# Kernel tuning notes

Hardware: AMD Instinct MI355X
Metric: run time of the kernel (lower is better)

## Reference

```python
import jax, jax.numpy as jnp
import numpy as np

ALPHA = 0.2  # LeakyReLU negative slope
EPS = 1e-6


def gam(x):
    # relu6(x+3)/3 + eps
    return jnp.clip(x + 3.0, 0.0, 6.0) / 3.0 + EPS


def leaky(x):
    return jnp.where(x >= 0, x, ALPHA * x)


def relu_bt(x):
    # threshold at detached inf-norm of input: min(leaky_relu(x), ||x||_inf)
    t = jax.lax.stop_gradient(jnp.max(jnp.abs(x)))
    return jnp.minimum(leaky(x), t)


def setup_inputs() -> dict:
    key = jax.random.key(0)
    ks = jax.random.split(key, 8)
    N, E, Din, Dout = 100000, 1600000, 256, 64
    return {
        "input": jax.random.normal(ks[0], (N, Din), dtype=jnp.float32),
        "edge": jax.random.randint(ks[1], (2, E), 0, N, dtype=jnp.int32),
        "W_high": jax.random.normal(ks[2], (Din, Dout), dtype=jnp.float32) * 0.06,
        "W_low": jax.random.normal(ks[3], (Din, Dout), dtype=jnp.float32) * 0.06,
        "a_high": jax.random.normal(ks[4], (1, 4 * Dout), dtype=jnp.float32) * 0.09,
        "a_low": jax.random.normal(ks[5], (1, 4 * Dout), dtype=jnp.float32) * 0.09,
        "c_high": jax.random.uniform(ks[6], (1, 1), dtype=jnp.float32),
        "c_low": jax.random.uniform(ks[7], (1, 1), dtype=jnp.float32),
    }


def reference(input, edge, W_high, W_low, a_high, a_low, c_high, c_low):
    N = input.shape[0]
    F = W_high.shape[1]
    src, dst = edge[0], edge[1]

    theta_high = gam(c_high) / 2.0  # [1,1]
    theta_low = gam(c_low) / 2.0

    h_high = relu_bt(input @ W_high)  # [N,F]
    h_low = relu_bt(input @ W_low)

    hh_s, hh_d = h_high[src], h_high[dst]  # [E,F]
    hl_s, hl_d = h_low[src], h_low[dst]

    ah = a_high[0]
    al = a_low[0]
    # a . [h_i, h_j, h_i+h_j, h_i-h_j] folded into per-endpoint coefficients
    # NOTE: original code uses h_high for the first two blocks of the LOW branch too.
    score_high = hh_s @ (ah[:F] + ah[2 * F:3 * F] + ah[3 * F:]) \
               + hh_d @ (ah[F:2 * F] + ah[2 * F:3 * F] - ah[3 * F:])  # [E]
    score_low = hh_s @ al[:F] + hh_d @ al[F:2 * F] \
              + hl_s @ (al[2 * F:3 * F] + al[3 * F:]) \
              + hl_d @ (al[2 * F:3 * F] - al[3 * F:])

    e_high = jnp.exp(-leaky(score_high / jnp.linalg.norm(a_high)))  # [E]
    e_low = jnp.exp(-leaky(score_low / jnp.linalg.norm(a_low)))

    # sparse COO spmm: rowsum and weighted aggregation
    rowsum_high = jax.ops.segment_sum(e_high, src, num_segments=N)[:, None]  # [N,1]
    rowsum_low = jax.ops.segment_sum(e_low, src, num_segments=N)[:, None]
    hp_high = jax.ops.segment_sum(e_high[:, None] * hh_d, src, num_segments=N)  # [N,F]
    hp_low = jax.ops.segment_sum(e_low[:, None] * hl_d, src, num_segments=N)

    hp_high = hp_high / (rowsum_high + theta_high)
    hp_low = hp_low / (rowsum_low + theta_low)

    # concat=True branch
    return relu_bt(jnp.concatenate([hp_high, hp_low], axis=1))  # [N,2F]
```

## Files before the change

kernel.cpp:

```cpp
#include <hip/hip_runtime.h>
#include <hip/hip_bf16.h>
#include <hip/hip_fp16.h>
#include <math.h>

typedef unsigned short ushort_t;
typedef unsigned int uint_t;
typedef __attribute__((ext_vector_type(8))) short short8;
typedef __attribute__((ext_vector_type(4))) float floatx4;
typedef __attribute__((ext_vector_type(4))) uint_t uintx4;
typedef __attribute__((ext_vector_type(4))) int intx4;

#define ALPHA 0.2f
#define CAP 64
#define NXCD 8
#define CPAD 16

__device__ __forceinline__ float leaky(float x) { return x >= 0.0f ? x : ALPHA * x; }

__device__ __forceinline__ float bf2f(ushort_t u) {
    union { uint_t i; float f; } v; v.i = ((uint_t)u) << 16; return v.f;
}
__device__ __forceinline__ float bflo(uint_t p) {
    union { uint_t i; float f; } v; v.i = p << 16; return v.f;
}
__device__ __forceinline__ float bfhi(uint_t p) {
    union { uint_t i; float f; } v; v.i = p & 0xffff0000u; return v.f;
}
__device__ __forceinline__ ushort_t f2bf(float f) {
    union { float f; uint_t i; } v; v.f = f;
    return (ushort_t)((v.i + 0x8000u) >> 16);
}
__device__ __forceinline__ uint_t pack_bf2(float a, float b) {
    union { float f; uint_t i; } ua, ub; ua.f = a; ub.f = b;
    return ((ua.i + 0x8000u) >> 16) | ((ub.i + 0x8000u) & 0xffff0000u);
}

__global__ void prep_wtrans_kernel(const float* __restrict__ Wh, const float* __restrict__ Wl,
                                   ushort_t* __restrict__ WTg,
                                   const float* __restrict__ ah, const float* __restrict__ al,
                                   const float* __restrict__ ch, const float* __restrict__ cl,
                                   float* __restrict__ coef, float* __restrict__ consts) {
    int t = threadIdx.x;
    if (blockIdx.x < 128) {
        int c = blockIdx.x;
        float v = (c < 64) ? Wh[t * 64 + c] : Wl[t * 64 + (c - 64)];
        WTg[c * 256 + t] = f2bf(v);
        return;
    }
    __shared__ float red[256];
    float va = ah[t];
    red[t] = va * va;
    __syncthreads();
    for (int s = 128; s > 0; s >>= 1) { if (t < s) red[t] += red[t + s]; __syncthreads(); }
    float sum_h = red[0];
    __syncthreads();
    float vb = al[t];
    red[t] = vb * vb;
    __syncthreads();
    for (int s = 128; s > 0; s >>= 1) { if (t < s) red[t] += red[t + s]; __syncthreads(); }
    float sum_l = red[0];

    if (t == 0) {
        consts[0] = 1.0f / sqrtf(sum_h);
        consts[1] = 1.0f / sqrtf(sum_l);
        float c = ch[0];
        float g = fminf(fmaxf(c + 3.0f, 0.0f), 6.0f) / 3.0f + 1e-6f;
        consts[2] = g * 0.5f;
        c = cl[0];
        g = fminf(fmaxf(c + 3.0f, 0.0f), 6.0f) / 3.0f + 1e-6f;
        consts[3] = g * 0.5f;
    }
    if (t < 128) {
        int f = t;
        float c0, c1, c2, c3;
        if (f < 64) {
            c0 = ah[f] + ah[128 + f] + ah[192 + f];
            c1 = ah[64 + f] + ah[128 + f] - ah[192 + f];
            c2 = al[f];
            c3 = al[64 + f];
        } else {
            int g = f - 64;
            c0 = 0.0f;
            c1 = 0.0f;
            c2 = al[128 + g] + al[192 + g];
            c3 = al[128 + g] - al[192 + g];
        }
        coef[0 * 128 + f] = c0;
        coef[1 * 128 + f] = c1;
        coef[2 * 128 + f] = c2;
        coef[3 * 128 + f] = c3;
    }
}

__global__ __launch_bounds__(256, 4) void gemm_kernel(const float* __restrict__ in,
                                                      const ushort_t* __restrict__ WTg,
                                                      const float* __restrict__ coef,
                                                      ushort_t* __restrict__ hcat,
                                                      float* __restrict__ s4, int N) {
    __shared__ ushort_t WT[128 * 128];
    __shared__ float coefS[512];
    int tid = threadIdx.x;
    for (int i = tid; i < 512; i += 256) coefS[i] = coef[i];

    int wave = tid >> 6, lane = tid & 63;
    int quad = lane >> 4, m16 = lane & 15;
    int rowbase = blockIdx.x * 64 + wave * 16;
    int arow = rowbase + m16;
    if (arow >= N) arow = N - 1;

    floatx4 acc[8];
#pragma unroll
    for (int ct = 0; ct < 8; ++ct) acc[ct] = (floatx4){0.0f, 0.0f, 0.0f, 0.0f};

    const uint4* WTg4 = (const uint4*)WTg;

#pragma unroll
    for (int kh = 0; kh < 2; ++kh) {
        if (kh) __syncthreads();
        for (int i = tid; i < 2048; i += 256) {
            int c = i >> 4, j = i & 15;
            int sj = j ^ (c & 7);
            uint4 v = WTg4[c * 32 + kh * 16 + j];
            *(uint4*)&WT[c * 128 + sj * 8] = v;
        }
        __syncthreads();
#pragma unroll
        for (int ks = 0; ks < 4; ++ks) {
            const floatx4* ap = (const floatx4*)(in + (size_t)arow * 256 + kh * 128 + ks * 32 + quad * 8);
            floatx4 a0 = __builtin_nontemporal_load(ap);
            floatx4 a1 = __builtin_nontemporal_load(ap + 1);
            union { uintx4 u; short8 s; } av;
            av.u[0] = pack_bf2(a0[0], a0[1]);
            av.u[1] = pack_bf2(a0[2], a0[3]);
            av.u[2] = pack_bf2(a1[0], a1[1]);
            av.u[3] = pack_bf2(a1[2], a1[3]);
#pragma unroll
            for (int ct = 0; ct < 8; ++ct) {
                int c = ct * 16 + m16;
                int sch = (ks * 4 + quad) ^ (c & 7);
                short8 b = *(const short8*)&WT[c * 128 + sch * 8];
                acc[ct] = __builtin_amdgcn_mfma_f32_16x16x32_bf16(av.s, b, acc[ct], 0, 0, 0);
            }
        }
    }

    float hv[8][4];
#pragma unroll
    for (int ct = 0; ct < 8; ++ct) {
#pragma unroll
        for (int r = 0; r < 4; ++r) {
            int row = rowbase + quad * 4 + r;
            float v = leaky(acc[ct][r]);
            hv[ct][r] = v;
            if (row < N) hcat[(size_t)row * 128 + ct * 16 + m16] = f2bf(v);
        }
    }
#pragma unroll
    for (int r = 0; r < 4; ++r) {
        int row = rowbase + quad * 4 + r;
        float p0 = 0, p1 = 0, p2 = 0, p3 = 0;
#pragma unroll
        for (int ct = 0; ct < 8; ++ct) {
            int c = ct * 16 + m16;
            float h = hv[ct][r];
            p0 += coefS[c] * h;
            p1 += coefS[128 + c] * h;
            p2 += coefS[256 + c] * h;
            p3 += coefS[384 + c] * h;
        }
#pragma unroll
        for (int off = 1; off < 16; off <<= 1) {
            p0 += __shfl_xor(p0, off);
            p1 += __shfl_xor(p1, off);
            p2 += __shfl_xor(p2, off);
            p3 += __shfl_xor(p3, off);
        }
        if (m16 == 0 && row < N) {
            floatx4 v = {p0, p1, p2, p3};
            *(floatx4*)&s4[(size_t)row * 4] = v;
        }
    }
}

__global__ __launch_bounds__(256) void scatter_kernel(const int* __restrict__ edge,
                                                      int* __restrict__ cursor,
                                                      uint_t* __restrict__ elist,
                                                      int E, int N) {
    int xcd = blockIdx.x & (NXCD - 1);
    int chunk = blockIdx.x >> 3;
    int TN = (N + NXCD - 1) / NXCD;
    int lo = xcd * TN;
    int hiN = lo + TN;
    int base = chunk * 2048 + threadIdx.x * 8;

    int sv[8], dv[8];
    if (base + 8 <= E) {
        intx4 s0 = *(const intx4*)(edge + base);
        intx4 s1 = *(const intx4*)(edge + base + 4);
        intx4 d0 = *(const intx4*)(edge + E + base);
        intx4 d1 = *(const intx4*)(edge + E + base + 4);
#pragma unroll
        for (int j = 0; j < 4; ++j) { sv[j] = s0[j]; sv[4 + j] = s1[j]; dv[j] = d0[j]; dv[4 + j] = d1[j]; }
    } else {
#pragma unroll
        for (int j = 0; j < 8; ++j) {
            bool ok = base + j < E;
            sv[j] = ok ? edge[base + j] : -1;
            dv[j] = ok ? edge[E + base + j] : 0;
        }
    }

    bool m[8];
    int pos[8];
#pragma unroll
    for (int j = 0; j < 8; ++j) m[j] = (sv[j] >= lo) & (sv[j] < hiN);
#pragma unroll
    for (int j = 0; j < 8; ++j) {
        pos[j] = 0;
        if (m[j]) pos[j] = atomicAdd(&cursor[(size_t)sv[j] * CPAD], 1);
    }
#pragma unroll
    for (int j = 0; j < 8; ++j) {
        if (m[j] && pos[j] < CAP) elist[(size_t)sv[j] * CAP + pos[j]] = (uint_t)dv[j];
    }
}

__global__ __launch_bounds__(256) void aggregate_kernel(const int* __restrict__ deg,
                                                        const uint_t* __restrict__ elist,
                                                        const ushort_t* __restrict__ hcat,
                                                        const float* __restrict__ s4,
                                                        const float* __restrict__ consts,
                                                        float* __restrict__ out, int N) {
    int w = (blockIdx.x * blockDim.x + threadIdx.x) >> 6;
    int lane = threadIdx.x & 63;
    if (w >= N) return;
    int d = deg[(size_t)w * CPAD];
    if (d > CAP) d = CAP;

    float s_own_h = s4[(size_t)w * 4 + 0];
    float s_own_l = s4[(size_t)w * 4 + 2];
    float inv_h = consts[0], inv_l = consts[1];
    int dst = 0;
    float wh = 0.0f, wl = 0.0f;
    if (lane < d) {
        dst = (int)elist[(size_t)w * CAP + lane];
        float4 sv = *(const float4*)&s4[(size_t)dst * 4];
        wh = __expf(-leaky((s_own_h + sv.y) * inv_h));
        wl = __expf(-leaky((s_own_l + sv.w) * inv_l));
    }
    uint_t wp = (uint_t)__half_as_ushort(__float2half(wh))
              | ((uint_t)__half_as_ushort(__float2half(wl)) << 16);
    float rsh = wh, rsl = wl;
#pragma unroll
    for (int off = 1; off < 64; off <<= 1) {
        rsh += __shfl_xor(rsh, off);
        rsl += __shfl_xor(rsl, off);
    }

    bool hi = lane < 32;
    int wsh = hi ? 0 : 16;
    const ushort_t* hbase = hcat + lane * 2;

    float2 c0 = {0.f, 0.f}, c1 = {0.f, 0.f}, c2 = {0.f, 0.f}, c3 = {0.f, 0.f};
    int j = 0;
    for (; j + 8 <= d; j += 8) {
        int dj[8];
        uint_t uj[8];
#pragma unroll
        for (int k = 0; k < 8; ++k) {
            dj[k] = __shfl(dst, j + k);
            uj[k] = (uint_t)__shfl((int)wp, j + k);
        }
        uint_t pj[8];
#pragma unroll
        for (int k = 0; k < 8; ++k) pj[k] = *(const uint_t*)&hbase[(size_t)dj[k] * 128];
#pragma unroll
        for (int k = 0; k < 8; ++k) {
            float wt = __half2float(__ushort_as_half((ushort_t)(uj[k] >> wsh)));
            float lo0 = bflo(pj[k]), hi1 = bfhi(pj[k]);
            if ((k & 3) == 0)      { c0.x += wt * lo0; c0.y += wt * hi1; }
            else if ((k & 3) == 1) { c1.x += wt * lo0; c1.y += wt * hi1; }
            else if ((k & 3) == 2) { c2.x += wt * lo0; c2.y += wt * hi1; }
            else                   { c3.x += wt * lo0; c3.y += wt * hi1; }
        }
    }
    for (; j < d; ++j) {
        int dj = __shfl(dst, j);
        uint_t uj = (uint_t)__shfl((int)wp, j);
        uint_t p = *(const uint_t*)&hbase[(size_t)dj * 128];
        float wt = __half2float(__ushort_as_half((ushort_t)(uj >> wsh)));
        c0.x += wt * bflo(p);
        c0.y += wt * bfhi(p);
    }

    float acc0 = (c0.x + c1.x) + (c2.x + c3.x);
    float acc1 = (c0.y + c1.y) + (c2.y + c3.y);
    float rsum = hi ? rsh : rsl;
    float theta = hi ? consts[2] : consts[3];
    float inv = 1.0f / (rsum + theta);
    float2 r;
    r.x = leaky(acc0 * inv);
    r.y = leaky(acc1 * inv);
    *(float2*)&out[(size_t)w * 128 + lane * 2] = r;
}

extern "C" void kernel_launch(void* const* d_in, const int* in_sizes, int n_in,
                              void* d_out, int out_size, void* d_ws, size_t ws_size,
                              hipStream_t stream) {
    const float* input = (const float*)d_in[0];
    const int* edge = (const int*)d_in[1];
    const float* Wh = (const float*)d_in[2];
    const float* Wl = (const float*)d_in[3];
    const float* ah = (const float*)d_in[4];
    const float* al = (const float*)d_in[5];
    const float* ch = (const float*)d_in[6];
    const float* cl = (const float*)d_in[7];
    int N = in_sizes[0] / 256;
    int E = in_sizes[1] / 2;
    float* out = (float*)d_out;

    char* ws = (char*)d_ws;
    size_t off = 0;
    uint_t* elist = (uint_t*)(ws + off);     off += (size_t)N * CAP * 4;
    ushort_t* hcat = (ushort_t*)(ws + off);  off += (size_t)N * 128 * 2;
    float* s4 = (float*)(ws + off);          off += (size_t)N * 4 * 4;
    int* cursor = (int*)(ws + off);          off += (size_t)N * CPAD * 4;
    ushort_t* WTg = (ushort_t*)(ws + off);   off += 128 * 256 * 2;
    float* coef = (float*)(ws + off);        off += 4 * 128 * 4;
    float* consts = (float*)(ws + off);      off += 64;

    hipMemsetAsync(cursor, 0, (size_t)N * CPAD * 4, stream);
    prep_wtrans_kernel<<<129, 256, 0, stream>>>(Wh, Wl, WTg, ah, al, ch, cl, coef, consts);
    gemm_kernel<<<(N + 63) / 64, 256, 0, stream>>>(input, WTg, coef, hcat, s4, N);
    int nchunks = (E + 2047) / 2048;
    scatter_kernel<<<nchunks * NXCD, 256, 0, stream>>>(edge, cursor, elist, E, N);
    aggregate_kernel<<<(N + 3) / 4, 256, 0, stream>>>(cursor, elist, hcat, s4, consts, out, N);
}
```

Before: 347.7 us.

## Slice hcat by 16-column groups and split aggregation across XCD-mapped blocks

The GEMM now stores hcat column-sliced, as 8 slabs of [N,16] bf16, in place of row-major [N,128]. Aggregation launches 8 blocks per node group, with blockIdx&7 selecting the slice, so on round-robin XCD dispatch each XCD gathers from a single 3.2MB slab that can stay in its L2. Each wave handles 8 edges at a time with 8 lanes per 32-byte row. The cost is 8x redundant edge-weight exp and elist/s4 reads, more blocks, and reliance on the block-to-XCD mapping.

```diff
diff --git a/kernel.cpp b/kernel.cpp
--- a/kernel.cpp
+++ b/kernel.cpp
@@ -152,7 +152,7 @@
             int row = rowbase + quad * 4 + r;
             float v = leaky(acc[ct][r]);
             hv[ct][r] = v;
-            if (row < N) hcat[(size_t)row * 128 + ct * 16 + m16] = f2bf(v);
+            if (row < N) hcat[((size_t)ct * N + row) * 16 + m16] = f2bf(v);
         }
     }
 #pragma unroll
@@ -231,77 +231,53 @@
                                                         const float* __restrict__ s4,
                                                         const float* __restrict__ consts,
                                                         float* __restrict__ out, int N) {
-    int w = (blockIdx.x * blockDim.x + threadIdx.x) >> 6;
+    int s = blockIdx.x & 7;
+    int g = blockIdx.x >> 3;
+    int wave = threadIdx.x >> 6;
     int lane = threadIdx.x & 63;
+    int w = g * 4 + wave;
     if (w >= N) return;
     int d = deg[(size_t)w * CPAD];
     if (d > CAP) d = CAP;
 
-    float s_own_h = s4[(size_t)w * 4 + 0];
-    float s_own_l = s4[(size_t)w * 4 + 2];
-    float inv_h = consts[0], inv_l = consts[1];
+    bool hib = s < 4;
+    float invn = hib ? consts[0] : consts[1];
+    float s_own = s4[(size_t)w * 4 + (hib ? 0 : 2)];
+
     int dst = 0;
-    float wh = 0.0f, wl = 0.0f;
+    float wt = 0.0f;
     if (lane < d) {
         dst = (int)elist[(size_t)w * CAP + lane];
-        float4 sv = *(const float4*)&s4[(size_t)dst * 4];
-        wh = __expf(-leaky((s_own_h + sv.y) * inv_h));
-        wl = __expf(-leaky((s_own_l + sv.w) * inv_l));
-    }
-    uint_t wp = (uint_t)__half_as_ushort(__float2half(wh))
-              | ((uint_t)__half_as_ushort(__float2half(wl)) << 16);
-    float rsh = wh, rsl = wl;
-#pragma unroll
-    for (int off = 1; off < 64; off <<= 1) {
-        rsh += __shfl_xor(rsh, off);
-        rsl += __shfl_xor(rsl, off);
-    }
-
-    bool hi = lane < 32;
-    int wsh = hi ? 0 : 16;
-    const ushort_t* hbase = hcat + lane * 2;
-
-    float2 c0 = {0.f, 0.f}, c1 = {0.f, 0.f}, c2 = {0.f, 0.f}, c3 = {0.f, 0.f};
-    int j = 0;
-    for (; j + 8 <= d; j += 8) {
-        int dj[8];
-        uint_t uj[8];
-#pragma unroll
-        for (int k = 0; k < 8; ++k) {
-            dj[k] = __shfl(dst, j + k);
-            uj[k] = (uint_t)__shfl((int)wp, j + k);
-        }
-        uint_t pj[8];
-#pragma unroll
-        for (int k = 0; k < 8; ++k) pj[k] = *(const uint_t*)&hbase[(size_t)dj[k] * 128];
-#pragma unroll
-        for (int k = 0; k < 8; ++k) {
-            float wt = __half2float(__ushort_as_half((ushort_t)(uj[k] >> wsh)));
-            float lo0 = bflo(pj[k]), hi1 = bfhi(pj[k]);
-            if ((k & 3) == 0)      { c0.x += wt * lo0; c0.y += wt * hi1; }
-            else if ((k & 3) == 1) { c1.x += wt * lo0; c1.y += wt * hi1; }
-            else if ((k & 3) == 2) { c2.x += wt * lo0; c2.y += wt * hi1; }
-            else                   { c3.x += wt * lo0; c3.y += wt * hi1; }
-        }
-    }
-    for (; j < d; ++j) {
+        float so = s4[(size_t)dst * 4 + (hib ? 1 : 3)];
+        wt = __expf(-leaky((s_own + so) * invn));
+    }
+
+    int e8 = lane >> 3, cp = lane & 7;
+    const ushort_t* hb = hcat + (size_t)s * N * 16 + cp * 2;
+    float accx = 0.0f, accy = 0.0f, rsum = 0.0f;
+    for (int jb = 0; jb < d; jb += 8) {
+        int j = jb + e8;
         int dj = __shfl(dst, j);
-        uint_t uj = (uint_t)__shfl((int)wp, j);
-        uint_t p = *(const uint_t*)&hbase[(size_t)dj * 128];
-        float wt = __half2float(__ushort_as_half((ushort_t)(uj >> wsh)));
-        c0.x += wt * bflo(p);
-        c0.y += wt * bfhi(p);
-    }
-
-    float acc0 = (c0.x + c1.x) + (c2.x + c3.x);
-    float acc1 = (c0.y + c1.y) + (c2.y + c3.y);
-    float rsum = hi ? rsh : rsl;
-    float theta = hi ? consts[2] : consts[3];
-    float inv = 1.0f / (rsum + theta);
-    float2 r;
-    r.x = leaky(acc0 * inv);
-    r.y = leaky(acc1 * inv);
-    *(float2*)&out[(size_t)w * 128 + lane * 2] = r;
+        float wj = __shfl(wt, j);
+        uint_t p = *(const uint_t*)&hb[(size_t)dj * 16];
+        accx += wj * bflo(p);
+        accy += wj * bfhi(p);
+        rsum += wj;
+    }
+#pragma unroll
+    for (int off = 8; off < 64; off <<= 1) {
+        accx += __shfl_xor(accx, off);
+        accy += __shfl_xor(accy, off);
+        rsum += __shfl_xor(rsum, off);
+    }
+    if (e8 == 0) {
+        float theta = hib ? consts[2] : consts[3];
+        float inv = 1.0f / (rsum + theta);
+        float2 r;
+        r.x = leaky(accx * inv);
+        r.y = leaky(accy * inv);
+        *(float2*)&out[(size_t)w * 128 + s * 16 + cp * 2] = r;
+    }
 }
 
 extern "C" void kernel_launch(void* const* d_in, const int* in_sizes, int n_in,
@@ -334,5 +310,6 @@
     gemm_kernel<<<(N + 63) / 64, 256, 0, stream>>>(input, WTg, coef, hcat, s4, N);
     int nchunks = (E + 2047) / 2048;
     scatter_kernel<<<nchunks * NXCD, 256, 0, stream>>>(edge, cursor, elist, E, N);
-    aggregate_kernel<<<(N + 3) / 4, 256, 0, stream>>>(cursor, elist, hcat, s4, consts, out, N);
-}
+    int Gagg = ((N + 3) / 4) * NXCD;
+    aggregate_kernel<<<Gagg, 256, 0, stream>>>(cursor, elist, hcat, s4, consts, out, N);
+}
```

Measured after the change: 544.0 us. 1.56x slower.

## Drop XCD-partitioned edge scatter and batch GEMM input loads ahead of MFMAs

Applied to the files above, without the earlier changes.

The scatter kernel no longer has each of eight XCD-aligned block groups re-read all edges and keep only sources in its node range. Each thread now handles four edges once, with blocks sized to cover E exactly, cutting edge reads eightfold. The cost is that atomics and elist writes from one node range are no longer confined to a single XCD's L2. Separately, the GEMM kernel issues all eight input vector loads for a K-half before converting and running MFMAs, to expose more memory-level parallelism at the cost of extra registers.

```diff
diff --git a/kernel.cpp b/kernel.cpp
--- a/kernel.cpp
+++ b/kernel.cpp
@@ -12,7 +12,6 @@
 
 #define ALPHA 0.2f
 #define CAP 64
-#define NXCD 8
 #define CPAD 16
 
 __device__ __forceinline__ float leaky(float x) { return x >= 0.0f ? x : ALPHA * x; }
@@ -124,16 +123,21 @@
             *(uint4*)&WT[c * 128 + sj * 8] = v;
         }
         __syncthreads();
+
+        const floatx4* apb = (const floatx4*)(in + (size_t)arow * 256 + kh * 128 + quad * 8);
+        floatx4 a[8];
 #pragma unroll
         for (int ks = 0; ks < 4; ++ks) {
-            const floatx4* ap = (const floatx4*)(in + (size_t)arow * 256 + kh * 128 + ks * 32 + quad * 8);
-            floatx4 a0 = __builtin_nontemporal_load(ap);
-            floatx4 a1 = __builtin_nontemporal_load(ap + 1);
+            a[2 * ks]     = __builtin_nontemporal_load(apb + ks * 8);
+            a[2 * ks + 1] = __builtin_nontemporal_load(apb + ks * 8 + 1);
+        }
+#pragma unroll
+        for (int ks = 0; ks < 4; ++ks) {
             union { uintx4 u; short8 s; } av;
-            av.u[0] = pack_bf2(a0[0], a0[1]);
-            av.u[1] = pack_bf2(a0[2], a0[3]);
-            av.u[2] = pack_bf2(a1[0], a1[1]);
-            av.u[3] = pack_bf2(a1[2], a1[3]);
+            av.u[0] = pack_bf2(a[2 * ks][0], a[2 * ks][1]);
+            av.u[1] = pack_bf2(a[2 * ks][2], a[2 * ks][3]);
+            av.u[2] = pack_bf2(a[2 * ks + 1][0], a[2 * ks + 1][1]);
+            av.u[3] = pack_bf2(a[2 * ks + 1][2], a[2 * ks + 1][3]);
 #pragma unroll
             for (int ct = 0; ct < 8; ++ct) {
                 int c = ct * 16 + m16;
@@ -185,43 +189,33 @@
 __global__ __launch_bounds__(256) void scatter_kernel(const int* __restrict__ edge,
                                                       int* __restrict__ cursor,
                                                       uint_t* __restrict__ elist,
-                                                      int E, int N) {
-    int xcd = blockIdx.x & (NXCD - 1);
-    int chunk = blockIdx.x >> 3;
-    int TN = (N + NXCD - 1) / NXCD;
-    int lo = xcd * TN;
-    int hiN = lo + TN;
-    int base = chunk * 2048 + threadIdx.x * 8;
-
-    int sv[8], dv[8];
-    if (base + 8 <= E) {
+                                                      int E) {
+    int base = (blockIdx.x * 256 + threadIdx.x) * 4;
+    if (base >= E) return;
+    int sv[4], dv[4];
+    bool m[4];
+    if (base + 4 <= E) {
         intx4 s0 = *(const intx4*)(edge + base);
-        intx4 s1 = *(const intx4*)(edge + base + 4);
         intx4 d0 = *(const intx4*)(edge + E + base);
-        intx4 d1 = *(const intx4*)(edge + E + base + 4);
-#pragma unroll
-        for (int j = 0; j < 4; ++j) { sv[j] = s0[j]; sv[4 + j] = s1[j]; dv[j] = d0[j]; dv[4 + j] = d1[j]; }
+#pragma unroll
+        for (int j = 0; j < 4; ++j) { sv[j] = s0[j]; dv[j] = d0[j]; m[j] = true; }
     } else {
 #pragma unroll
-        for (int j = 0; j < 8; ++j) {
-            bool ok = base + j < E;
-            sv[j] = ok ? edge[base + j] : -1;
-            dv[j] = ok ? edge[E + base + j] : 0;
-        }
-    }
-
-    bool m[8];
-    int pos[8];
-#pragma unroll
-    for (int j = 0; j < 8; ++j) m[j] = (sv[j] >= lo) & (sv[j] < hiN);
-#pragma unroll
-    for (int j = 0; j < 8; ++j) {
-        pos[j] = 0;
+        for (int j = 0; j < 4; ++j) {
+            m[j] = base + j < E;
+            sv[j] = m[j] ? edge[base + j] : 0;
+            dv[j] = m[j] ? edge[E + base + j] : 0;
+        }
+    }
+    int pos[4];
+#pragma unroll
+    for (int j = 0; j < 4; ++j) {
+        pos[j] = CAP;
         if (m[j]) pos[j] = atomicAdd(&cursor[(size_t)sv[j] * CPAD], 1);
     }
 #pragma unroll
-    for (int j = 0; j < 8; ++j) {
-        if (m[j] && pos[j] < CAP) elist[(size_t)sv[j] * CAP + pos[j]] = (uint_t)dv[j];
+    for (int j = 0; j < 4; ++j) {
+        if (pos[j] < CAP) elist[(size_t)sv[j] * CAP + pos[j]] = (uint_t)dv[j];
     }
 }
 
@@ -332,7 +326,7 @@
     hipMemsetAsync(cursor, 0, (size_t)N * CPAD * 4, stream);
     prep_wtrans_kernel<<<129, 256, 0, stream>>>(Wh, Wl, WTg, ah, al, ch, cl, coef, consts);
     gemm_kernel<<<(N + 63) / 64, 256, 0, stream>>>(input, WTg, coef, hcat, s4, N);
-    int nchunks = (E + 2047) / 2048;
-    scatter_kernel<<<nchunks * NXCD, 256, 0, stream>>>(edge, cursor, elist, E, N);
+    int Gscat = (E + 1023) / 1024;
+    scatter_kernel<<<Gscat, 256, 0, stream>>>(edge, cursor, elist, E);
     aggregate_kernel<<<(N + 3) / 4, 256, 0, stream>>>(cursor, elist, hcat, s4, consts, out, N);
 }
```

Measured after the change: 394.0 us. +13.3%, slower.

## Compact cursor array, grid-stride scatter, and batch GEMM A loads

Applied to the files above, without the earlier changes.

Removes the 16-int padding per cursor so the counter array and its memset shrink, at the cost of more atomic contention on shared cache lines. The scatter kernel becomes a grid-stride loop over a fixed 2048-block grid, which cuts the number of blocks that each re-read all edges only to filter by XCD. In the GEMM, all eight A-row loads for a K-half are issued before any packing or MFMA work so more memory requests are in flight, at the cost of extra registers.

```diff
diff --git a/kernel.cpp b/kernel.cpp
--- a/kernel.cpp
+++ b/kernel.cpp
@@ -13,7 +13,6 @@
 #define ALPHA 0.2f
 #define CAP 64
 #define NXCD 8
-#define CPAD 16
 
 __device__ __forceinline__ float leaky(float x) { return x >= 0.0f ? x : ALPHA * x; }
 
@@ -124,16 +123,21 @@
             *(uint4*)&WT[c * 128 + sj * 8] = v;
         }
         __syncthreads();
+
+        const floatx4* apb = (const floatx4*)(in + (size_t)arow * 256 + kh * 128 + quad * 8);
+        floatx4 a[8];
 #pragma unroll
         for (int ks = 0; ks < 4; ++ks) {
-            const floatx4* ap = (const floatx4*)(in + (size_t)arow * 256 + kh * 128 + ks * 32 + quad * 8);
-            floatx4 a0 = __builtin_nontemporal_load(ap);
-            floatx4 a1 = __builtin_nontemporal_load(ap + 1);
+            a[2 * ks]     = __builtin_nontemporal_load(apb + ks * 8);
+            a[2 * ks + 1] = __builtin_nontemporal_load(apb + ks * 8 + 1);
+        }
+#pragma unroll
+        for (int ks = 0; ks < 4; ++ks) {
             union { uintx4 u; short8 s; } av;
-            av.u[0] = pack_bf2(a0[0], a0[1]);
-            av.u[1] = pack_bf2(a0[2], a0[3]);
-            av.u[2] = pack_bf2(a1[0], a1[1]);
-            av.u[3] = pack_bf2(a1[2], a1[3]);
+            av.u[0] = pack_bf2(a[2 * ks][0], a[2 * ks][1]);
+            av.u[1] = pack_bf2(a[2 * ks][2], a[2 * ks][3]);
+            av.u[2] = pack_bf2(a[2 * ks + 1][0], a[2 * ks + 1][1]);
+            av.u[3] = pack_bf2(a[2 * ks + 1][2], a[2 * ks + 1][3]);
 #pragma unroll
             for (int ct = 0; ct < 8; ++ct) {
                 int c = ct * 16 + m16;
@@ -187,41 +191,43 @@
                                                       uint_t* __restrict__ elist,
                                                       int E, int N) {
     int xcd = blockIdx.x & (NXCD - 1);
-    int chunk = blockIdx.x >> 3;
+    int cidx = blockIdx.x >> 3;
+    int nch = gridDim.x >> 3;
     int TN = (N + NXCD - 1) / NXCD;
     int lo = xcd * TN;
     int hiN = lo + TN;
-    int base = chunk * 2048 + threadIdx.x * 8;
-
-    int sv[8], dv[8];
-    if (base + 8 <= E) {
-        intx4 s0 = *(const intx4*)(edge + base);
-        intx4 s1 = *(const intx4*)(edge + base + 4);
-        intx4 d0 = *(const intx4*)(edge + E + base);
-        intx4 d1 = *(const intx4*)(edge + E + base + 4);
-#pragma unroll
-        for (int j = 0; j < 4; ++j) { sv[j] = s0[j]; sv[4 + j] = s1[j]; dv[j] = d0[j]; dv[4 + j] = d1[j]; }
-    } else {
+
+    for (int base = (cidx * 256 + threadIdx.x) * 8; base < E; base += nch * 256 * 8) {
+        int sv[8], dv[8];
+        if (base + 8 <= E) {
+            intx4 s0 = *(const intx4*)(edge + base);
+            intx4 s1 = *(const intx4*)(edge + base + 4);
+            intx4 d0 = *(const intx4*)(edge + E + base);
+            intx4 d1 = *(const intx4*)(edge + E + base + 4);
+#pragma unroll
+            for (int j = 0; j < 4; ++j) { sv[j] = s0[j]; sv[4 + j] = s1[j]; dv[j] = d0[j]; dv[4 + j] = d1[j]; }
+        } else {
+#pragma unroll
+            for (int j = 0; j < 8; ++j) {
+                bool ok = base + j < E;
+                sv[j] = ok ? edge[base + j] : -1;
+                dv[j] = ok ? edge[E + base + j] : 0;
+            }
+        }
+
+        bool m[8];
+        int pos[8];
+#pragma unroll
+        for (int j = 0; j < 8; ++j) m[j] = (sv[j] >= lo) & (sv[j] < hiN);
 #pragma unroll
         for (int j = 0; j < 8; ++j) {
-            bool ok = base + j < E;
-            sv[j] = ok ? edge[base + j] : -1;
-            dv[j] = ok ? edge[E + base + j] : 0;
-        }
-    }
-
-    bool m[8];
-    int pos[8];
-#pragma unroll
-    for (int j = 0; j < 8; ++j) m[j] = (sv[j] >= lo) & (sv[j] < hiN);
-#pragma unroll
-    for (int j = 0; j < 8; ++j) {
-        pos[j] = 0;
-        if (m[j]) pos[j] = atomicAdd(&cursor[(size_t)sv[j] * CPAD], 1);
-    }
-#pragma unroll
-    for (int j = 0; j < 8; ++j) {
-        if (m[j] && pos[j] < CAP) elist[(size_t)sv[j] * CAP + pos[j]] = (uint_t)dv[j];
+            pos[j] = 0;
+            if (m[j]) pos[j] = atomicAdd(&cursor[sv[j]], 1);
+        }
+#pragma unroll
+        for (int j = 0; j < 8; ++j) {
+            if (m[j] && pos[j] < CAP) elist[(size_t)sv[j] * CAP + pos[j]] = (uint_t)dv[j];
+        }
     }
 }
 
@@ -234,7 +240,7 @@
     int w = (blockIdx.x * blockDim.x + threadIdx.x) >> 6;
     int lane = threadIdx.x & 63;
     if (w >= N) return;
-    int d = deg[(size_t)w * CPAD];
+    int d = deg[w];
     if (d > CAP) d = CAP;
 
     float s_own_h = s4[(size_t)w * 4 + 0];
@@ -324,15 +330,14 @@
     uint_t* elist = (uint_t*)(ws + off);     off += (size_t)N * CAP * 4;
     ushort_t* hcat = (ushort_t*)(ws + off);  off += (size_t)N * 128 * 2;
     float* s4 = (float*)(ws + off);          off += (size_t)N * 4 * 4;
-    int* cursor = (int*)(ws + off);          off += (size_t)N * CPAD * 4;
+    int* cursor = (int*)(ws + off);          off += (size_t)N * 4;
     ushort_t* WTg = (ushort_t*)(ws + off);   off += 128 * 256 * 2;
     float* coef = (float*)(ws + off);        off += 4 * 128 * 4;
     float* consts = (float*)(ws + off);      off += 64;
 
-    hipMemsetAsync(cursor, 0, (size_t)N * CPAD * 4, stream);
+    hipMemsetAsync(cursor, 0, (size_t)N * 4, stream);
     prep_wtrans_kernel<<<129, 256, 0, stream>>>(Wh, Wl, WTg, ah, al, ch, cl, coef, consts);
     gemm_kernel<<<(N + 63) / 64, 256, 0, stream>>>(input, WTg, coef, hcat, s4, N);
-    int nchunks = (E + 2047) / 2048;
-    scatter_kernel<<<nchunks * NXCD, 256, 0, stream>>>(edge, cursor, elist, E, N);
+    scatter_kernel<<<2048, 256, 0, stream>>>(edge, cursor, elist, E, N);
     aggregate_kernel<<<(N + 3) / 4, 256, 0, stream>>>(cursor, elist, hcat, s4, consts, out, N);
 }
```

New measurement: 348.2 us. No clear change (+0.2%).
